# Kernel optimization log

Measured on AMD Instinct MI355X. Metric: run time of the kernel, lower is better.

## Reference

```python
import jax, jax.numpy as jnp
import numpy as np

B, I, H = 16384, 512, 512


def setup_inputs() -> dict:
    key = jax.random.key(0)
    ks = jax.random.split(key, 9)
    std = 1.0 / np.sqrt(H)
    u = lambda k, shape: jax.random.uniform(k, shape, jnp.float32, -std, std)
    return {
        "input": jax.random.normal(ks[0], (B, I), jnp.float32),
        "h_prev": jax.random.normal(ks[1], (B, H), jnp.float32),
        "c_prev": jax.random.normal(ks[2], (B, H), jnp.float32),
        "m_prev": jax.random.normal(ks[3], (B, H), jnp.float32),
        "n_prev": jnp.ones((B, H), jnp.float32),
        "Wxh": u(ks[4], (4 * H, I)),
        "bxh": u(ks[5], (4 * H,)),
        "Whh": u(ks[6], (4 * H, H)),
        "bhh": u(ks[7], (4 * H,)),
    }


def reference(input, h_prev, c_prev, m_prev, n_prev, Wxh, bxh, Whh, bhh):
    # gates = xh(input) + hh(h_prev) -> [B, 4H]
    gates = input @ Wxh.T + bxh + h_prev @ Whh.T + bhh
    ig, fg, zg, og = jnp.split(gates, 4, axis=1)
    z_t = jnp.tanh(zg)
    o_t = jax.nn.sigmoid(og)
    # log-space stabilizer: log(exp(fg)) = fg, log(exp(ig)) = ig
    m_t = jnp.maximum(fg + m_prev, ig)
    i_t = jnp.exp(ig - m_t)
    f_t = jnp.exp(fg + m_prev - m_t)
    c_t = f_t * c_prev + i_t * z_t
    n_t = f_t * n_prev + i_t
    h_t = o_t * (c_t / n_t)
    return (h_t, c_t, m_t, n_t)
```

## Files before the change

kernel.cpp:

```cpp
#include <hip/hip_runtime.h>

#define Bsz 16384
#define Isz 512
#define Hsz 512
#define Ksz 1024
#define N4H 2048

#define BM 128
#define BK 64

typedef __bf16 bf16x8 __attribute__((ext_vector_type(8)));
typedef __bf16 bf16x4 __attribute__((ext_vector_type(4)));
typedef float  f32x4  __attribute__((ext_vector_type(4)));

__device__ __forceinline__ void async_copy16(const void* g, void* l) {
    __builtin_amdgcn_global_load_lds(
        (__attribute__((address_space(1))) void*)g,
        (__attribute__((address_space(3))) void*)l,
        16, 0, 0);
}

__global__ void pack_all(const float* __restrict__ x, const float* __restrict__ h,
                         const float* __restrict__ Wxh, const float* __restrict__ Whh,
                         const float* __restrict__ bxh, const float* __restrict__ bhh,
                         __bf16* __restrict__ Aq, __bf16* __restrict__ Bq,
                         float* __restrict__ bias) {
    if (blockIdx.x < 16384) {
        int idx = blockIdx.x * 256 + threadIdx.x;
        int e   = idx << 2;
        int row = e >> 10, col = e & 1023;
        const float4 v = (col < Isz)
            ? *(const float4*)(x + (size_t)row * Isz + col)
            : *(const float4*)(h + (size_t)row * Hsz + (col - Isz));
        bf16x4 o = { (__bf16)v.x, (__bf16)v.y, (__bf16)v.z, (__bf16)v.w };
        *(bf16x4*)(Aq + (size_t)e) = o;
    } else {
        int idx = (blockIdx.x - 16384) * 256 + threadIdx.x;
        int p   = idx >> 8;
        int k   = (idx & 255) << 2;
        int nb  = p >> 7, n = p & 127;
        int wn  = n >> 6, t = (n >> 4) & 3, c = n & 15;
        int orow = t * Hsz + nb * 32 + wn * 16 + c;
        const float4 v = (k < Isz)
            ? *(const float4*)(Wxh + (size_t)orow * Isz + k)
            : *(const float4*)(Whh + (size_t)orow * Hsz + (k - Isz));
        bf16x4 o = { (__bf16)v.x, (__bf16)v.y, (__bf16)v.z, (__bf16)v.w };
        *(bf16x4*)(Bq + (size_t)p * Ksz + k) = o;
        if ((idx & 255) == 0) bias[p] = bxh[orow] + bhh[orow];
    }
}

__global__ __launch_bounds__(256, 4) void slstm_gemm(
    const __bf16* __restrict__ Aq, const __bf16* __restrict__ Bq,
    const float* __restrict__ bias,
    const float* __restrict__ c_prev, const float* __restrict__ m_prev,
    const float* __restrict__ n_prev, float* __restrict__ out) {

    __shared__ __bf16 As[BM * BK];
    __shared__ __bf16 Bs[BM * BK];

    const int tid  = threadIdx.x;
    const int w    = tid >> 6;
    const int lane = tid & 63;
    const int wm   = w & 1;
    const int wn   = w >> 1;
    const int bm   = blockIdx.x;
    const int nb   = blockIdx.y;

    const __bf16* Ag = Aq + (size_t)bm * BM * Ksz;
    const __bf16* Bg = Bq + (size_t)nb * BM * Ksz;

    f32x4 acc[4][4];
    const f32x4 zero = {0.f, 0.f, 0.f, 0.f};
#pragma unroll
    for (int mi = 0; mi < 4; ++mi)
#pragma unroll
        for (int ni = 0; ni < 4; ++ni) acc[mi][ni] = zero;

    const int srow = (lane >> 3);
    const int scol = ((lane & 7) ^ srow) * 8;

    for (int k0 = 0; k0 < Ksz; k0 += BK) {
        __syncthreads();
#pragma unroll
        for (int i = 0; i < 4; ++i) {
            const int chunk = w * 4 + i;
            const int row   = chunk * 8 + srow;
            async_copy16(Ag + (size_t)row * Ksz + k0 + scol, (char*)As + chunk * 1024);
            async_copy16(Bg + (size_t)row * Ksz + k0 + scol, (char*)Bs + chunk * 1024);
        }
        __syncthreads();

#pragma unroll
        for (int kk = 0; kk < 2; ++kk) {
            bf16x8 af[4], bf[4];
#pragma unroll
            for (int mi = 0; mi < 4; ++mi) {
                const int r = wm * 64 + mi * 16 + (lane & 15);
                const int p = (kk * 4 + (lane >> 4)) ^ (r & 7);
                af[mi] = *(const bf16x8*)(As + r * BK + p * 8);
            }
#pragma unroll
            for (int ni = 0; ni < 4; ++ni) {
                const int r = wn * 64 + ni * 16 + (lane & 15);
                const int p = (kk * 4 + (lane >> 4)) ^ (r & 7);
                bf[ni] = *(const bf16x8*)(Bs + r * BK + p * 8);
            }
#pragma unroll
            for (int mi = 0; mi < 4; ++mi)
#pragma unroll
                for (int ni = 0; ni < 4; ++ni)
                    acc[mi][ni] = __builtin_amdgcn_mfma_f32_16x16x32_bf16(
                        af[mi], bf[ni], acc[mi][ni], 0, 0, 0);
        }
    }

    const int hidx = nb * 32 + wn * 16 + (lane & 15);
    const int quad = lane >> 4;

    float bsv[4];
#pragma unroll
    for (int ni = 0; ni < 4; ++ni)
        bsv[ni] = bias[nb * 128 + wn * 64 + ni * 16 + (lane & 15)];

    const size_t BH = (size_t)Bsz * Hsz;

#pragma unroll
    for (int mi = 0; mi < 4; ++mi) {
        const int mbase = bm * 128 + wm * 64 + mi * 16 + quad * 4;
#pragma unroll
        for (int r = 0; r < 4; ++r) {
            const int m = mbase + r;
            const size_t off = (size_t)m * Hsz + hidx;
            const float ig = acc[mi][0][r] + bsv[0];
            const float fg = acc[mi][1][r] + bsv[1];
            const float zg = acc[mi][2][r] + bsv[2];
            const float og = acc[mi][3][r] + bsv[3];
            const float cp = c_prev[off];
            const float mp = m_prev[off];
            const float np = n_prev[off];
            const float zt = tanhf(zg);
            const float ot = 1.f / (1.f + expf(-og));
            const float fm = fg + mp;
            const float mt = fmaxf(fm, ig);
            const float it = expf(ig - mt);
            const float ft = expf(fm - mt);
            const float ct = ft * cp + it * zt;
            const float nt = ft * np + it;
            const float ht = ot * (ct / nt);
            out[off]          = ht;
            out[BH + off]     = ct;
            out[2 * BH + off] = mt;
            out[3 * BH + off] = nt;
        }
    }
}

extern "C" void kernel_launch(void* const* d_in, const int* in_sizes, int n_in,
                              void* d_out, int out_size, void* d_ws, size_t ws_size,
                              hipStream_t stream) {
    const float* input  = (const float*)d_in[0];
    const float* h_prev = (const float*)d_in[1];
    const float* c_prev = (const float*)d_in[2];
    const float* m_prev = (const float*)d_in[3];
    const float* n_prev = (const float*)d_in[4];
    const float* Wxh    = (const float*)d_in[5];
    const float* bxh    = (const float*)d_in[6];
    const float* Whh    = (const float*)d_in[7];
    const float* bhh    = (const float*)d_in[8];
    float* out = (float*)d_out;

    __bf16* Aq   = (__bf16*)d_ws;
    __bf16* Bq   = (__bf16*)((char*)d_ws + (size_t)Bsz * Ksz * 2);
    float*  bias = (float*)((char*)d_ws + (size_t)Bsz * Ksz * 2 + (size_t)N4H * Ksz * 2);

    pack_all<<<16384 + 2048, 256, 0, stream>>>(input, h_prev, Wxh, Whh, bxh, bhh,
                                               Aq, Bq, bias);

    dim3 grid(Bsz / BM, Hsz / 32);
    slstm_gemm<<<grid, 256, 0, stream>>>(Aq, Bq, bias, c_prev, m_prev, n_prev, out);
}
```

Baseline: 344.6 us.

## Fuse activation fp32-to-bf16 conversion into GEMM A-tile loading

Removes the separate packing pass that converted input and h_prev into a bf16 workspace; the GEMM now reads fp32 activations directly, converts them in registers and writes swizzled bf16 into LDS. Only the weights are still prepacked. This avoids a large workspace write and read, but each column block now re-reads the fp32 activations at twice the bytes, and the loads are synchronous rather than async-to-LDS, which can expose latency in the main loop.

```diff
diff --git a/kernel.cpp b/kernel.cpp
--- a/kernel.cpp
+++ b/kernel.cpp
@@ -20,39 +20,26 @@
         16, 0, 0);
 }
 
-__global__ void pack_all(const float* __restrict__ x, const float* __restrict__ h,
-                         const float* __restrict__ Wxh, const float* __restrict__ Whh,
-                         const float* __restrict__ bxh, const float* __restrict__ bhh,
-                         __bf16* __restrict__ Aq, __bf16* __restrict__ Bq,
-                         float* __restrict__ bias) {
-    if (blockIdx.x < 16384) {
-        int idx = blockIdx.x * 256 + threadIdx.x;
-        int e   = idx << 2;
-        int row = e >> 10, col = e & 1023;
-        const float4 v = (col < Isz)
-            ? *(const float4*)(x + (size_t)row * Isz + col)
-            : *(const float4*)(h + (size_t)row * Hsz + (col - Isz));
-        bf16x4 o = { (__bf16)v.x, (__bf16)v.y, (__bf16)v.z, (__bf16)v.w };
-        *(bf16x4*)(Aq + (size_t)e) = o;
-    } else {
-        int idx = (blockIdx.x - 16384) * 256 + threadIdx.x;
-        int p   = idx >> 8;
-        int k   = (idx & 255) << 2;
-        int nb  = p >> 7, n = p & 127;
-        int wn  = n >> 6, t = (n >> 4) & 3, c = n & 15;
-        int orow = t * Hsz + nb * 32 + wn * 16 + c;
-        const float4 v = (k < Isz)
-            ? *(const float4*)(Wxh + (size_t)orow * Isz + k)
-            : *(const float4*)(Whh + (size_t)orow * Hsz + (k - Isz));
-        bf16x4 o = { (__bf16)v.x, (__bf16)v.y, (__bf16)v.z, (__bf16)v.w };
-        *(bf16x4*)(Bq + (size_t)p * Ksz + k) = o;
-        if ((idx & 255) == 0) bias[p] = bxh[orow] + bhh[orow];
-    }
+__global__ void pack_w(const float* __restrict__ Wxh, const float* __restrict__ Whh,
+                       const float* __restrict__ bxh, const float* __restrict__ bhh,
+                       __bf16* __restrict__ Bq, float* __restrict__ bias) {
+    int idx = blockIdx.x * 256 + threadIdx.x;
+    int p   = idx >> 8;
+    int k   = (idx & 255) << 2;
+    int nb  = p >> 7, n = p & 127;
+    int wn  = n >> 6, t = (n >> 4) & 3, c = n & 15;
+    int orow = t * Hsz + nb * 32 + wn * 16 + c;
+    const float4 v = (k < Isz)
+        ? *(const float4*)(Wxh + (size_t)orow * Isz + k)
+        : *(const float4*)(Whh + (size_t)orow * Hsz + (k - Isz));
+    bf16x4 o = { (__bf16)v.x, (__bf16)v.y, (__bf16)v.z, (__bf16)v.w };
+    *(bf16x4*)(Bq + (size_t)p * Ksz + k) = o;
+    if ((idx & 255) == 0) bias[p] = bxh[orow] + bhh[orow];
 }
 
 __global__ __launch_bounds__(256, 4) void slstm_gemm(
-    const __bf16* __restrict__ Aq, const __bf16* __restrict__ Bq,
-    const float* __restrict__ bias,
+    const float* __restrict__ input, const float* __restrict__ h_prev,
+    const __bf16* __restrict__ Bq, const float* __restrict__ bias,
     const float* __restrict__ c_prev, const float* __restrict__ m_prev,
     const float* __restrict__ n_prev, float* __restrict__ out) {
 
@@ -67,7 +54,6 @@
     const int bm   = blockIdx.x;
     const int nb   = blockIdx.y;
 
-    const __bf16* Ag = Aq + (size_t)bm * BM * Ksz;
     const __bf16* Bg = Bq + (size_t)nb * BM * Ksz;
 
     f32x4 acc[4][4];
@@ -80,13 +66,35 @@
     const int srow = (lane >> 3);
     const int scol = ((lane & 7) ^ srow) * 8;
 
+    const int g2  = tid & 7;
+    const int ar0 = tid >> 3;
+
     for (int k0 = 0; k0 < Ksz; k0 += BK) {
+        const float* Asrc = (k0 < Isz)
+            ? (input  + (size_t)(bm * BM) * Isz + k0)
+            : (h_prev + (size_t)(bm * BM) * Hsz + (k0 - Isz));
+        float4 va[4], vb[4];
+#pragma unroll
+        for (int i = 0; i < 4; ++i) {
+            const int row = i * 32 + ar0;
+            va[i] = *(const float4*)(Asrc + (size_t)row * 512 + g2 * 8);
+            vb[i] = *(const float4*)(Asrc + (size_t)row * 512 + g2 * 8 + 4);
+        }
+
         __syncthreads();
+
+#pragma unroll
+        for (int i = 0; i < 4; ++i) {
+            const int row = i * 32 + ar0;
+            bf16x8 o = { (__bf16)va[i].x, (__bf16)va[i].y, (__bf16)va[i].z, (__bf16)va[i].w,
+                         (__bf16)vb[i].x, (__bf16)vb[i].y, (__bf16)vb[i].z, (__bf16)vb[i].w };
+            const int p = g2 ^ (row & 7);
+            *(bf16x8*)(As + row * BK + p * 8) = o;
+        }
 #pragma unroll
         for (int i = 0; i < 4; ++i) {
             const int chunk = w * 4 + i;
             const int row   = chunk * 8 + srow;
-            async_copy16(Ag + (size_t)row * Ksz + k0 + scol, (char*)As + chunk * 1024);
             async_copy16(Bg + (size_t)row * Ksz + k0 + scol, (char*)Bs + chunk * 1024);
         }
         __syncthreads();
@@ -170,13 +178,12 @@
     const float* bhh    = (const float*)d_in[8];
     float* out = (float*)d_out;
 
-    __bf16* Aq   = (__bf16*)d_ws;
-    __bf16* Bq   = (__bf16*)((char*)d_ws + (size_t)Bsz * Ksz * 2);
-    float*  bias = (float*)((char*)d_ws + (size_t)Bsz * Ksz * 2 + (size_t)N4H * Ksz * 2);
+    __bf16* Bq   = (__bf16*)d_ws;
+    float*  bias = (float*)((char*)d_ws + (size_t)N4H * Ksz * 2);
 
-    pack_all<<<16384 + 2048, 256, 0, stream>>>(input, h_prev, Wxh, Whh, bxh, bhh,
-                                               Aq, Bq, bias);
+    pack_w<<<(N4H * Ksz / 4) / 256, 256, 0, stream>>>(Wxh, Whh, bxh, bhh, Bq, bias);
 
     dim3 grid(Bsz / BM, Hsz / 32);
-    slstm_gemm<<<grid, 256, 0, stream>>>(Aq, Bq, bias, c_prev, m_prev, n_prev, out);
+    slstm_gemm<<<grid, 256, 0, stream>>>(input, h_prev, Bq, bias,
+                                         c_prev, m_prev, n_prev, out);
 }
```

New measurement: 360.1 us. 4.5% more time.
